# Optimization experiments

Measured on AMD Instinct MI355X. Metric: run time of the kernel, lower is better.

Reference implementation:

```python
import jax, jax.numpy as jnp
import numpy as np

B, K, U, I, D = 16384, 64, 100000, 100000, 256

def setup_inputs() -> dict:
    key = jax.random.key(0)
    k1, k2, k3, k4, k5, k6, k7, k8 = jax.random.split(key, 8)
    return {
        "nodes_u": jax.random.randint(k1, (B,), 0, U),
        "nodes_v": jax.random.randint(k2, (B,), 0, I),
        "neighbors": jax.random.randint(k3, (B, K), 0, U),
        "neighbor_counts": jax.random.randint(k4, (B,), 0, K + 1),
        "u2e": jax.random.normal(k5, (U, D), dtype=jnp.float32),
        "v2e": jax.random.normal(k6, (I, D), dtype=jnp.float32),
        "W": jax.random.normal(k7, (D, 2 * D), dtype=jnp.float32) * 0.05,  # torch Linear weight [out, in]
        "b": jax.random.normal(k8, (D,), dtype=jnp.float32) * 0.05,
    }

def reference(nodes_u, nodes_v, neighbors, neighbor_counts, u2e, v2e, W, b):
    # self embeddings [B, D]
    self_emb = u2e[nodes_u]
    # gather padded neighbor embeddings [B, K, D]
    neib_emb = u2e[neighbors]
    k_ = neighbors.shape[1]
    mask = jnp.arange(k_)[None, :] < neighbor_counts[:, None]          # [B, K] valid-neighbor mask
    nsum = jnp.einsum('bkd,bk->bd', neib_emb, mask.astype(neib_emb.dtype))
    cnt = jnp.maximum(neighbor_counts, 1).astype(self_emb.dtype)[:, None]
    nmean = nsum / cnt                                                  # mean-pool over valid neighbors
    cat = jnp.concatenate([self_emb, nmean], axis=1)                    # [B, 2D]
    proj = cat @ W.T + b                                                # Linear(2D -> D)
    # users with no neighbors use raw self embedding (matches `if len(neibs) > 0` branch)
    uemb = jnp.where((neighbor_counts > 0)[:, None], proj, self_emb)
    scores = jnp.sum(uemb * v2e[nodes_v], axis=1)                       # [B]
    return scores
```

## Files before the change

### kernel.cpp

```cpp
#include <hip/hip_runtime.h>
#include <hip/hip_fp16.h>

#define B_ROWS   16384
#define K_NB     64
#define U_ROWS   100000
#define D_DIM    256
#define TWO_D    512
#define R_BLK    8
#define THREADS  256

typedef float f32x2_t __attribute__((ext_vector_type(2)));

#if __has_builtin(__builtin_amdgcn_cvt_pk_f32_fp8) && __has_builtin(__builtin_amdgcn_cvt_pk_fp8_f32)
#define FP8_HW 1
#else
#define FP8_HW 0
#include <hip/hip_fp8.h>
#endif

__device__ __forceinline__ unsigned pack4_fp8(float a, float b, float c, float d) {
#if FP8_HW
    int v = 0;
    v = __builtin_amdgcn_cvt_pk_fp8_f32(a, b, v, false);
    v = __builtin_amdgcn_cvt_pk_fp8_f32(c, d, v, true);
    return (unsigned)v;
#else
    __hip_fp8_e4m3 x0(a), x1(b), x2(c), x3(d);
    return (unsigned)x0.__x | ((unsigned)x1.__x << 8)
         | ((unsigned)x2.__x << 16) | ((unsigned)x3.__x << 24);
#endif
}

__device__ __forceinline__ float4 unpack4_fp8(unsigned u) {
#if FP8_HW
    const f32x2_t lo = __builtin_amdgcn_cvt_pk_f32_fp8((int)u, false);
    const f32x2_t hi = __builtin_amdgcn_cvt_pk_f32_fp8((int)u, true);
    return make_float4(lo[0], lo[1], hi[0], hi[1]);
#else
    __hip_fp8_e4m3 x0, x1, x2, x3;
    x0.__x = u & 0xff; x1.__x = (u >> 8) & 0xff;
    x2.__x = (u >> 16) & 0xff; x3.__x = (u >> 24) & 0xff;
    return make_float4((float)x0, (float)x1, (float)x2, (float)x3);
#endif
}

__global__ __launch_bounds__(256)
void cvt_u2e_fp8(const float* __restrict__ src, uint2* __restrict__ dst, int n8) {
    const int i = blockIdx.x * 256 + threadIdx.x;
    if (i >= n8) return;
    const float4 a = ((const float4*)src)[2 * i];
    const float4 b = ((const float4*)src)[2 * i + 1];
    uint2 o;
    o.x = pack4_fp8(a.x, a.y, a.z, a.w);
    o.y = pack4_fp8(b.x, b.y, b.z, b.w);
    dst[i] = o;
}

__global__ __launch_bounds__(THREADS, 4)
void easyrec_fused_q(const int* __restrict__ nodes_u,
                     const int* __restrict__ nodes_v,
                     const int* __restrict__ neighbors,
                     const int* __restrict__ neighbor_counts,
                     const float* __restrict__ u2e,
                     const unsigned char* __restrict__ u8,
                     const float* __restrict__ v2e,
                     const float* __restrict__ W,
                     const float* __restrict__ bias,
                     float* __restrict__ out)
{
    __shared__ __align__(16) int   nbr_lds[R_BLK * K_NB];
    __shared__ __align__(16) float cat_lds[R_BLK][TWO_D];
    __shared__ float red_lds[R_BLK * 4];
    __shared__ float selfdot_lds[R_BLK];
    __shared__ float bdot_lds[R_BLK];

    const int t    = threadIdx.x;
    const int wave = t >> 6;
    const int lane = t & 63;
    const int row0 = blockIdx.x * R_BLK;

    nbr_lds[t]           = neighbors[(size_t)row0 * K_NB + t];
    nbr_lds[t + THREADS] = neighbors[(size_t)row0 * K_NB + t + THREADS];
    __syncthreads();

    const unsigned colb = (unsigned)lane * 16u;
    const unsigned colq = (unsigned)lane * 4u;

    {
        const float4 b4 = *(const float4*)((const char*)bias + colb);
        #pragma unroll
        for (int rr = 0; rr < 2; ++rr) {
            const int r   = wave + rr * 4;
            const int row = row0 + r;
            const int nu  = __builtin_amdgcn_readfirstlane(nodes_u[row]);
            const int nv  = __builtin_amdgcn_readfirstlane(nodes_v[row]);
            const float4 self4 = *(const float4*)((const char*)u2e + (((size_t)nu) << 10) + colb);
            const float4 v4    = *(const float4*)((const char*)v2e + (((size_t)nv) << 10) + colb);
            *(float4*)(&cat_lds[r][4 * lane]) = self4;
            float sv = self4.x * v4.x + self4.y * v4.y + self4.z * v4.z + self4.w * v4.w;
            float bv = b4.x * v4.x + b4.y * v4.y + b4.z * v4.z + b4.w * v4.w;
            #pragma unroll
            for (int off = 32; off > 0; off >>= 1) {
                sv += __shfl_xor(sv, off, 64);
                bv += __shfl_xor(bv, off, 64);
            }
            if (lane == 0) { selfdot_lds[r] = sv; bdot_lds[r] = bv; }
        }
    }

    const int rowA = row0 + wave, rowB = rowA + 4;
    const int cntA = __builtin_amdgcn_readfirstlane(neighbor_counts[rowA]);
    const int cntB = __builtin_amdgcn_readfirstlane(neighbor_counts[rowB]);
    const int itA = (cntA + 7) >> 3;
    const int itB = (cntB + 7) >> 3;
    const int itMin = itA < itB ? itA : itB;
    const int itMax = itA > itB ? itA : itB;
    const int baseA = wave * K_NB;
    const int baseB = baseA + 4 * K_NB;

#define LOADQ8(P, BASE, KK)                                                         \
    const int4 P##ia = *(const int4*)&nbr_lds[(BASE) + (KK)];                       \
    const int4 P##ib = *(const int4*)&nbr_lds[(BASE) + (KK) + 4];                   \
    const unsigned P##n0 = *(const unsigned*)(u8 + (((unsigned)P##ia.x) << 8) + colq); \
    const unsigned P##n1 = *(const unsigned*)(u8 + (((unsigned)P##ia.y) << 8) + colq); \
    const unsigned P##n2 = *(const unsigned*)(u8 + (((unsigned)P##ia.z) << 8) + colq); \
    const unsigned P##n3 = *(const unsigned*)(u8 + (((unsigned)P##ia.w) << 8) + colq); \
    const unsigned P##n4 = *(const unsigned*)(u8 + (((unsigned)P##ib.x) << 8) + colq); \
    const unsigned P##n5 = *(const unsigned*)(u8 + (((unsigned)P##ib.y) << 8) + colq); \
    const unsigned P##n6 = *(const unsigned*)(u8 + (((unsigned)P##ib.z) << 8) + colq); \
    const unsigned P##n7 = *(const unsigned*)(u8 + (((unsigned)P##ib.w) << 8) + colq);

#define ACCQ1(P, N, ACC, M)                                                         \
    {                                                                               \
        const float4 f = unpack4_fp8(P##N);                                         \
        ACC.x += (M) * f.x; ACC.y += (M) * f.y;                                     \
        ACC.z += (M) * f.z; ACC.w += (M) * f.w;                                     \
    }

#define ACCQ8(P, ACC, CNT, KK)                                                      \
    {                                                                               \
        const float m0 = ((KK) + 0 < (CNT)) ? 1.f : 0.f;                            \
        const float m1 = ((KK) + 1 < (CNT)) ? 1.f : 0.f;                            \
        const float m2 = ((KK) + 2 < (CNT)) ? 1.f : 0.f;                            \
        const float m3 = ((KK) + 3 < (CNT)) ? 1.f : 0.f;                            \
        const float m4 = ((KK) + 4 < (CNT)) ? 1.f : 0.f;                            \
        const float m5 = ((KK) + 5 < (CNT)) ? 1.f : 0.f;                            \
        const float m6 = ((KK) + 6 < (CNT)) ? 1.f : 0.f;                            \
        const float m7 = ((KK) + 7 < (CNT)) ? 1.f : 0.f;                            \
        ACCQ1(P, n0, ACC, m0) ACCQ1(P, n1, ACC, m1)                                 \
        ACCQ1(P, n2, ACC, m2) ACCQ1(P, n3, ACC, m3)                                 \
        ACCQ1(P, n4, ACC, m4) ACCQ1(P, n5, ACC, m5)                                 \
        ACCQ1(P, n6, ACC, m6) ACCQ1(P, n7, ACC, m7)                                 \
    }

    float4 accA = make_float4(0.f, 0.f, 0.f, 0.f);
    float4 accB = make_float4(0.f, 0.f, 0.f, 0.f);

    for (int i = 0; i < itMin; ++i) {
        const int k = i << 3;
        LOADQ8(A, baseA, k)
        LOADQ8(B, baseB, k)
        ACCQ8(A, accA, cntA, k)
        ACCQ8(B, accB, cntB, k)
    }
    if (itMin < itMax) {
        const bool Along = itA > itB;
        const int  cntL  = Along ? cntA : cntB;
        const int  baseL = Along ? baseA : baseB;
        float4 accL = make_float4(0.f, 0.f, 0.f, 0.f);
        for (int i = itMin; i < itMax; ++i) {
            const int k = i << 3;
            LOADQ8(L, baseL, k)
            ACCQ8(L, accL, cntL, k)
        }
        if (Along) {
            accA.x += accL.x; accA.y += accL.y; accA.z += accL.z; accA.w += accL.w;
        } else {
            accB.x += accL.x; accB.y += accL.y; accB.z += accL.z; accB.w += accL.w;
        }
    }
#undef LOADQ8
#undef ACCQ8
#undef ACCQ1

    {
        const float invA = 1.0f / (float)(cntA > 0 ? cntA : 1);
        const float invB = 1.0f / (float)(cntB > 0 ? cntB : 1);
        *(float4*)(&cat_lds[wave][D_DIM + 4 * lane]) =
            make_float4(accA.x * invA, accA.y * invA, accA.z * invA, accA.w * invA);
        *(float4*)(&cat_lds[wave + 4][D_DIM + 4 * lane]) =
            make_float4(accB.x * invB, accB.y * invB, accB.z * invB, accB.w * invB);
    }
    __syncthreads();

    unsigned voff[R_BLK];
    #pragma unroll
    for (int r = 0; r < R_BLK; ++r) {
        const int nv = __builtin_amdgcn_readfirstlane(nodes_v[row0 + r]);
        voff[r] = ((unsigned)nv) << 10;
    }

    float2 acc2[R_BLK];
    #pragma unroll
    for (int r = 0; r < R_BLK; ++r) acc2[r] = make_float2(0.f, 0.f);

    const unsigned tb8 = (unsigned)t * 8u;
    for (int d = 0; d < D_DIM; d += 4) {
        float4 vq[R_BLK];
        #pragma unroll
        for (int r = 0; r < R_BLK; ++r)
            vq[r] = *(const float4*)((const char*)v2e + voff[r] + (unsigned)d * 4u);

        #pragma unroll
        for (int dd = 0; dd < 4; ++dd) {
            const float2 wq = *(const float2*)((const char*)W + (((unsigned)(d + dd)) << 11) + tb8);
            #pragma unroll
            for (int r = 0; r < R_BLK; ++r) {
                const float vs = (dd == 0) ? vq[r].x : (dd == 1) ? vq[r].y
                               : (dd == 2) ? vq[r].z : vq[r].w;
                acc2[r].x += wq.x * vs;
                acc2[r].y += wq.y * vs;
            }
        }
    }

    #pragma unroll
    for (int r = 0; r < R_BLK; ++r) {
        const float2 c2 = *(const float2*)(&cat_lds[r][2 * t]);
        float p = c2.x * acc2[r].x + c2.y * acc2[r].y;
        #pragma unroll
        for (int off = 32; off > 0; off >>= 1) p += __shfl_xor(p, off, 64);
        if (lane == 0) red_lds[r * 4 + wave] = p;
    }
    __syncthreads();

    if (t < R_BLK) {
        const int row = row0 + t;
        const int cnt = neighbor_counts[row];
        float s;
        if (cnt > 0) {
            s = red_lds[t * 4 + 0] + red_lds[t * 4 + 1]
              + red_lds[t * 4 + 2] + red_lds[t * 4 + 3] + bdot_lds[t];
        } else {
            s = selfdot_lds[t];
        }
        out[row] = s;
    }
}

__global__ __launch_bounds__(THREADS, 4)
void easyrec_fused_f(const int* __restrict__ nodes_u,
                     const int* __restrict__ nodes_v,
                     const int* __restrict__ neighbors,
                     const int* __restrict__ neighbor_counts,
                     const float* __restrict__ u2e,
                     const float* __restrict__ v2e,
                     const float* __restrict__ W,
                     const float* __restrict__ bias,
                     float* __restrict__ out)
{
    __shared__ __align__(16) int   nbr_lds[R_BLK * K_NB];
    __shared__ __align__(16) float cat_lds[R_BLK][TWO_D];
    __shared__ float red_lds[R_BLK * 4];
    __shared__ float selfdot_lds[R_BLK];
    __shared__ float bdot_lds[R_BLK];

    const int t    = threadIdx.x;
    const int wave = t >> 6;
    const int lane = t & 63;
    const int row0 = blockIdx.x * R_BLK;

    nbr_lds[t]           = neighbors[(size_t)row0 * K_NB + t];
    nbr_lds[t + THREADS] = neighbors[(size_t)row0 * K_NB + t + THREADS];
    __syncthreads();

    for (int rr = 0; rr < 2; ++rr) {
        const int r   = wave + rr * 4;
        const int row = row0 + r;
        const int nu  = __builtin_amdgcn_readfirstlane(nodes_u[row]);
        const int nv  = __builtin_amdgcn_readfirstlane(nodes_v[row]);
        const int cnt = __builtin_amdgcn_readfirstlane(neighbor_counts[row]);

        const float4 self4 = *(const float4*)(u2e + (size_t)nu * D_DIM + 4 * lane);
        const float4 v4    = *(const float4*)(v2e + (size_t)nv * D_DIM + 4 * lane);
        const float4 b4    = *(const float4*)(bias + 4 * lane);

        float4 acc = make_float4(0.f, 0.f, 0.f, 0.f);
        const int base = r * K_NB;
        const int kmax = (cnt + 7) & ~7;
        for (int k = 0; k < kmax; k += 8) {
            const int4 ia = *(const int4*)&nbr_lds[base + k];
            const int4 ib = *(const int4*)&nbr_lds[base + k + 4];
            const float4 n0 = *(const float4*)(u2e + (size_t)ia.x * D_DIM + 4 * lane);
            const float4 n1 = *(const float4*)(u2e + (size_t)ia.y * D_DIM + 4 * lane);
            const float4 n2 = *(const float4*)(u2e + (size_t)ia.z * D_DIM + 4 * lane);
            const float4 n3 = *(const float4*)(u2e + (size_t)ia.w * D_DIM + 4 * lane);
            const float4 n4 = *(const float4*)(u2e + (size_t)ib.x * D_DIM + 4 * lane);
            const float4 n5 = *(const float4*)(u2e + (size_t)ib.y * D_DIM + 4 * lane);
            const float4 n6 = *(const float4*)(u2e + (size_t)ib.z * D_DIM + 4 * lane);
            const float4 n7 = *(const float4*)(u2e + (size_t)ib.w * D_DIM + 4 * lane);
            const float m0 = (k + 0 < cnt) ? 1.f : 0.f;
            const float m1 = (k + 1 < cnt) ? 1.f : 0.f;
            const float m2 = (k + 2 < cnt) ? 1.f : 0.f;
            const float m3 = (k + 3 < cnt) ? 1.f : 0.f;
            const float m4 = (k + 4 < cnt) ? 1.f : 0.f;
            const float m5 = (k + 5 < cnt) ? 1.f : 0.f;
            const float m6 = (k + 6 < cnt) ? 1.f : 0.f;
            const float m7 = (k + 7 < cnt) ? 1.f : 0.f;
            acc.x += n0.x*m0 + n1.x*m1 + n2.x*m2 + n3.x*m3 + n4.x*m4 + n5.x*m5 + n6.x*m6 + n7.x*m7;
            acc.y += n0.y*m0 + n1.y*m1 + n2.y*m2 + n3.y*m3 + n4.y*m4 + n5.y*m5 + n6.y*m6 + n7.y*m7;
            acc.z += n0.z*m0 + n1.z*m1 + n2.z*m2 + n3.z*m3 + n4.z*m4 + n5.z*m5 + n6.z*m6 + n7.z*m7;
            acc.w += n0.w*m0 + n1.w*m1 + n2.w*m2 + n3.w*m3 + n4.w*m4 + n5.w*m5 + n6.w*m6 + n7.w*m7;
        }
        const float inv = 1.0f / (float)(cnt > 0 ? cnt : 1);
        *(float4*)(&cat_lds[r][4 * lane])         = self4;
        *(float4*)(&cat_lds[r][D_DIM + 4 * lane]) =
            make_float4(acc.x * inv, acc.y * inv, acc.z * inv, acc.w * inv);

        float sv = self4.x * v4.x + self4.y * v4.y + self4.z * v4.z + self4.w * v4.w;
        float bv = b4.x * v4.x + b4.y * v4.y + b4.z * v4.z + b4.w * v4.w;
        #pragma unroll
        for (int off = 32; off > 0; off >>= 1) {
            sv += __shfl_xor(sv, off, 64);
            bv += __shfl_xor(bv, off, 64);
        }
        if (lane == 0) { selfdot_lds[r] = sv; bdot_lds[r] = bv; }
    }
    __syncthreads();

    const float* vrow[R_BLK];
    #pragma unroll
    for (int r = 0; r < R_BLK; ++r) {
        const int nv = __builtin_amdgcn_readfirstlane(nodes_v[row0 + r]);
        vrow[r] = v2e + (size_t)nv * D_DIM;
    }

    float2 acc2[R_BLK];
    #pragma unroll
    for (int r = 0; r < R_BLK; ++r) acc2[r] = make_float2(0.f, 0.f);

    for (int d = 0; d < D_DIM; d += 4) {
        float4 vq[R_BLK];
        #pragma unroll
        for (int r = 0; r < R_BLK; ++r) vq[r] = *(const float4*)(vrow[r] + d);
        #pragma unroll
        for (int dd = 0; dd < 4; ++dd) {
            const float2 wq = *(const float2*)(W + (size_t)(d + dd) * TWO_D + 2 * t);
            #pragma unroll
            for (int r = 0; r < R_BLK; ++r) {
                const float vs = (dd == 0) ? vq[r].x : (dd == 1) ? vq[r].y
                               : (dd == 2) ? vq[r].z : vq[r].w;
                acc2[r].x += wq.x * vs;
                acc2[r].y += wq.y * vs;
            }
        }
    }

    #pragma unroll
    for (int r = 0; r < R_BLK; ++r) {
        const float2 c2 = *(const float2*)(&cat_lds[r][2 * t]);
        float p = c2.x * acc2[r].x + c2.y * acc2[r].y;
        #pragma unroll
        for (int off = 32; off > 0; off >>= 1) p += __shfl_xor(p, off, 64);
        if (lane == 0) red_lds[r * 4 + wave] = p;
    }
    __syncthreads();

    if (t < R_BLK) {
        const int row = row0 + t;
        const int cnt = neighbor_counts[row];
        float s;
        if (cnt > 0) {
            s = red_lds[t * 4 + 0] + red_lds[t * 4 + 1]
              + red_lds[t * 4 + 2] + red_lds[t * 4 + 3] + bdot_lds[t];
        } else {
            s = selfdot_lds[t];
        }
        out[row] = s;
    }
}

extern "C" void kernel_launch(void* const* d_in, const int* in_sizes, int n_in,
                              void* d_out, int out_size, void* d_ws, size_t ws_size,
                              hipStream_t stream) {
    const int*   nodes_u         = (const int*)d_in[0];
    const int*   nodes_v         = (const int*)d_in[1];
    const int*   neighbors       = (const int*)d_in[2];
    const int*   neighbor_counts = (const int*)d_in[3];
    const float* u2e             = (const float*)d_in[4];
    const float* v2e             = (const float*)d_in[5];
    const float* W               = (const float*)d_in[6];
    const float* bias            = (const float*)d_in[7];
    float*       out             = (float*)d_out;

    const size_t need = (size_t)U_ROWS * D_DIM;
    const int blocks = B_ROWS / R_BLK;

    if (d_ws != nullptr && ws_size >= need) {
        unsigned char* u8 = (unsigned char*)d_ws;
        const int n8 = U_ROWS * D_DIM / 8;
        const int cblocks = (n8 + 255) / 256;
        cvt_u2e_fp8<<<cblocks, 256, 0, stream>>>(u2e, (uint2*)u8, n8);
        easyrec_fused_q<<<blocks, THREADS, 0, stream>>>(
            nodes_u, nodes_v, neighbors, neighbor_counts, u2e, u8, v2e, W, bias, out);
    } else {
        easyrec_fused_f<<<blocks, THREADS, 0, stream>>>(
            nodes_u, nodes_v, neighbors, neighbor_counts, u2e, v2e, W, bias, out);
    }
}
```

Baseline: 302.6 us.

## Specialize waves: two gather neighbors while two compute W-projection concurrently

```diff
diff --git a/kernel.cpp b/kernel.cpp
--- a/kernel.cpp
+++ b/kernel.cpp
@@ -70,7 +70,7 @@
 {
     __shared__ __align__(16) int   nbr_lds[R_BLK * K_NB];
     __shared__ __align__(16) float cat_lds[R_BLK][TWO_D];
-    __shared__ float red_lds[R_BLK * 4];
+    __shared__ float red_lds[R_BLK * 2];
     __shared__ float selfdot_lds[R_BLK];
     __shared__ float bdot_lds[R_BLK];
 
@@ -83,40 +83,31 @@
     nbr_lds[t + THREADS] = neighbors[(size_t)row0 * K_NB + t + THREADS];
     __syncthreads();
 
-    const unsigned colb = (unsigned)lane * 16u;
-    const unsigned colq = (unsigned)lane * 4u;
-
-    {
-        const float4 b4 = *(const float4*)((const char*)bias + colb);
-        #pragma unroll
-        for (int rr = 0; rr < 2; ++rr) {
-            const int r   = wave + rr * 4;
-            const int row = row0 + r;
-            const int nu  = __builtin_amdgcn_readfirstlane(nodes_u[row]);
-            const int nv  = __builtin_amdgcn_readfirstlane(nodes_v[row]);
-            const float4 self4 = *(const float4*)((const char*)u2e + (((size_t)nu) << 10) + colb);
-            const float4 v4    = *(const float4*)((const char*)v2e + (((size_t)nv) << 10) + colb);
-            *(float4*)(&cat_lds[r][4 * lane]) = self4;
-            float sv = self4.x * v4.x + self4.y * v4.y + self4.z * v4.z + self4.w * v4.w;
-            float bv = b4.x * v4.x + b4.y * v4.y + b4.z * v4.z + b4.w * v4.w;
+    if (wave < 2) {
+        const unsigned colb = (unsigned)lane * 16u;
+        const unsigned colq = (unsigned)lane * 4u;
+
+        {
+            const float4 b4 = *(const float4*)((const char*)bias + colb);
             #pragma unroll
-            for (int off = 32; off > 0; off >>= 1) {
-                sv += __shfl_xor(sv, off, 64);
-                bv += __shfl_xor(bv, off, 64);
+            for (int rr = 0; rr < 4; ++rr) {
+                const int r   = wave * 2 + (rr & 1) + (rr >> 1) * 4;
+                const int row = row0 + r;
+                const int nu  = __builtin_amdgcn_readfirstlane(nodes_u[row]);
+                const int nv  = __builtin_amdgcn_readfirstlane(nodes_v[row]);
+                const float4 self4 = *(const float4*)((const char*)u2e + (((size_t)nu) << 10) + colb);
+                const float4 v4    = *(const float4*)((const char*)v2e + (((size_t)nv) << 10) + colb);
+                *(float4*)(&cat_lds[r][4 * lane]) = self4;
+                float sv = self4.x * v4.x + self4.y * v4.y + self4.z * v4.z + self4.w * v4.w;
+                float bv = b4.x * v4.x + b4.y * v4.y + b4.z * v4.z + b4.w * v4.w;
+                #pragma unroll
+                for (int off = 32; off > 0; off >>= 1) {
+                    sv += __shfl_xor(sv, off, 64);
+                    bv += __shfl_xor(bv, off, 64);
+                }
+                if (lane == 0) { selfdot_lds[r] = sv; bdot_lds[r] = bv; }
             }
-            if (lane == 0) { selfdot_lds[r] = sv; bdot_lds[r] = bv; }
-        }
-    }
-
-    const int rowA = row0 + wave, rowB = rowA + 4;
-    const int cntA = __builtin_amdgcn_readfirstlane(neighbor_counts[rowA]);
-    const int cntB = __builtin_amdgcn_readfirstlane(neighbor_counts[rowB]);
-    const int itA = (cntA + 7) >> 3;
-    const int itB = (cntB + 7) >> 3;
-    const int itMin = itA < itB ? itA : itB;
-    const int itMax = itA > itB ? itA : itB;
-    const int baseA = wave * K_NB;
-    const int baseB = baseA + 4 * K_NB;
+        }
 
 #define LOADQ8(P, BASE, KK)                                                         \
     const int4 P##ia = *(const int4*)&nbr_lds[(BASE) + (KK)];                       \
@@ -153,85 +144,103 @@
         ACCQ1(P, n6, ACC, m6) ACCQ1(P, n7, ACC, m7)                                 \
     }
 
-    float4 accA = make_float4(0.f, 0.f, 0.f, 0.f);
-    float4 accB = make_float4(0.f, 0.f, 0.f, 0.f);
-
-    for (int i = 0; i < itMin; ++i) {
-        const int k = i << 3;
-        LOADQ8(A, baseA, k)
-        LOADQ8(B, baseB, k)
-        ACCQ8(A, accA, cntA, k)
-        ACCQ8(B, accB, cntB, k)
-    }
-    if (itMin < itMax) {
-        const bool Along = itA > itB;
-        const int  cntL  = Along ? cntA : cntB;
-        const int  baseL = Along ? baseA : baseB;
-        float4 accL = make_float4(0.f, 0.f, 0.f, 0.f);
-        for (int i = itMin; i < itMax; ++i) {
-            const int k = i << 3;
-            LOADQ8(L, baseL, k)
-            ACCQ8(L, accL, cntL, k)
-        }
-        if (Along) {
-            accA.x += accL.x; accA.y += accL.y; accA.z += accL.z; accA.w += accL.w;
-        } else {
-            accB.x += accL.x; accB.y += accL.y; accB.z += accL.z; accB.w += accL.w;
-        }
-    }
+        for (int pp = 0; pp < 2; ++pp) {
+            const int rA = wave * 2 + pp;
+            const int rB = rA + 4;
+            const int cntA = __builtin_amdgcn_readfirstlane(neighbor_counts[row0 + rA]);
+            const int cntB = __builtin_amdgcn_readfirstlane(neighbor_counts[row0 + rB]);
+            const int itA = (cntA + 7) >> 3;
+            const int itB = (cntB + 7) >> 3;
+            const int itMin = itA < itB ? itA : itB;
+            const int itMax = itA > itB ? itA : itB;
+            const int baseA = rA * K_NB;
+            const int baseB = rB * K_NB;
+
+            float4 accA = make_float4(0.f, 0.f, 0.f, 0.f);
+            float4 accB = make_float4(0.f, 0.f, 0.f, 0.f);
+
+            for (int i = 0; i < itMin; ++i) {
+                const int k = i << 3;
+                LOADQ8(A, baseA, k)
+                LOADQ8(B, baseB, k)
+                ACCQ8(A, accA, cntA, k)
+                ACCQ8(B, accB, cntB, k)
+            }
+            if (itMin < itMax) {
+                const bool Along = itA > itB;
+                const int  cntL  = Along ? cntA : cntB;
+                const int  baseL = Along ? baseA : baseB;
+                float4 accL = make_float4(0.f, 0.f, 0.f, 0.f);
+                for (int i = itMin; i < itMax; ++i) {
+                    const int k = i << 3;
+                    LOADQ8(L, baseL, k)
+                    ACCQ8(L, accL, cntL, k)
+                }
+                if (Along) {
+                    accA.x += accL.x; accA.y += accL.y; accA.z += accL.z; accA.w += accL.w;
+                } else {
+                    accB.x += accL.x; accB.y += accL.y; accB.z += accL.z; accB.w += accL.w;
+                }
+            }
+
+            const float invA = 1.0f / (float)(cntA > 0 ? cntA : 1);
+            const float invB = 1.0f / (float)(cntB > 0 ? cntB : 1);
+            *(float4*)(&cat_lds[rA][D_DIM + 4 * lane]) =
+                make_float4(accA.x * invA, accA.y * invA, accA.z * invA, accA.w * invA);
+            *(float4*)(&cat_lds[rB][D_DIM + 4 * lane]) =
+                make_float4(accB.x * invB, accB.y * invB, accB.z * invB, accB.w * invB);
+        }
 #undef LOADQ8
 #undef ACCQ8
 #undef ACCQ1
-
-    {
-        const float invA = 1.0f / (float)(cntA > 0 ? cntA : 1);
-        const float invB = 1.0f / (float)(cntB > 0 ? cntB : 1);
-        *(float4*)(&cat_lds[wave][D_DIM + 4 * lane]) =
-            make_float4(accA.x * invA, accA.y * invA, accA.z * invA, accA.w * invA);
-        *(float4*)(&cat_lds[wave + 4][D_DIM + 4 * lane]) =
-            make_float4(accB.x * invB, accB.y * invB, accB.z * invB, accB.w * invB);
-    }
-    __syncthreads();
-
-    unsigned voff[R_BLK];
-    #pragma unroll
-    for (int r = 0; r < R_BLK; ++r) {
-        const int nv = __builtin_amdgcn_readfirstlane(nodes_v[row0 + r]);
-        voff[r] = ((unsigned)nv) << 10;
-    }
-
-    float2 acc2[R_BLK];
-    #pragma unroll
-    for (int r = 0; r < R_BLK; ++r) acc2[r] = make_float2(0.f, 0.f);
-
-    const unsigned tb8 = (unsigned)t * 8u;
-    for (int d = 0; d < D_DIM; d += 4) {
-        float4 vq[R_BLK];
-        #pragma unroll
-        for (int r = 0; r < R_BLK; ++r)
-            vq[r] = *(const float4*)((const char*)v2e + voff[r] + (unsigned)d * 4u);
-
-        #pragma unroll
-        for (int dd = 0; dd < 4; ++dd) {
-            const float2 wq = *(const float2*)((const char*)W + (((unsigned)(d + dd)) << 11) + tb8);
+    } else {
+        const int tm = t - 128;
+        unsigned voff[R_BLK];
+        #pragma unroll
+        for (int r = 0; r < R_BLK; ++r) {
+            const int nv = __builtin_amdgcn_readfirstlane(nodes_v[row0 + r]);
+            voff[r] = ((unsigned)nv) << 10;
+        }
+
+        float4 acc4[R_BLK];
+        #pragma unroll
+        for (int r = 0; r < R_BLK; ++r) acc4[r] = make_float4(0.f, 0.f, 0.f, 0.f);
+
+        const unsigned tb16 = (unsigned)tm * 16u;
+        for (int d = 0; d < D_DIM; d += 4) {
+            float4 vq[R_BLK];
             #pragma unroll
-            for (int r = 0; r < R_BLK; ++r) {
-                const float vs = (dd == 0) ? vq[r].x : (dd == 1) ? vq[r].y
-                               : (dd == 2) ? vq[r].z : vq[r].w;
-                acc2[r].x += wq.x * vs;
-                acc2[r].y += wq.y * vs;
+            for (int r = 0; r < R_BLK; ++r)
+                vq[r] = *(const float4*)((const char*)v2e + voff[r] + (unsigned)d * 4u);
+
+            #pragma unroll
+            for (int dd = 0; dd < 4; ++dd) {
+                const float4 w4 = *(const float4*)((const char*)W + (((unsigned)(d + dd)) << 11) + tb16);
+                #pragma unroll
+                for (int r = 0; r < R_BLK; ++r) {
+                    const float vs = (dd == 0) ? vq[r].x : (dd == 1) ? vq[r].y
+                                   : (dd == 2) ? vq[r].z : vq[r].w;
+                    acc4[r].x += w4.x * vs;
+                    acc4[r].y += w4.y * vs;
+                    acc4[r].z += w4.z * vs;
+                    acc4[r].w += w4.w * vs;
+                }
             }
         }
-    }
-
-    #pragma unroll
-    for (int r = 0; r < R_BLK; ++r) {
-        const float2 c2 = *(const float2*)(&cat_lds[r][2 * t]);
-        float p = c2.x * acc2[r].x + c2.y * acc2[r].y;
-        #pragma unroll
-        for (int off = 32; off > 0; off >>= 1) p += __shfl_xor(p, off, 64);
-        if (lane == 0) red_lds[r * 4 + wave] = p;
-    }
+        __syncthreads();
+
+        #pragma unroll
+        for (int r = 0; r < R_BLK; ++r) {
+            const float4 c4 = *(const float4*)(&cat_lds[r][4 * tm]);
+            float p = c4.x * acc4[r].x + c4.y * acc4[r].y
+                    + c4.z * acc4[r].z + c4.w * acc4[r].w;
+            #pragma unroll
+            for (int off = 32; off > 0; off >>= 1) p += __shfl_xor(p, off, 64);
+            if (lane == 0) red_lds[r * 2 + (wave - 2)] = p;
+        }
+    }
+
+    if (wave < 2) __syncthreads();
     __syncthreads();
 
     if (t < R_BLK) {
@@ -239,8 +248,7 @@
         const int cnt = neighbor_counts[row];
         float s;
         if (cnt > 0) {
-            s = red_lds[t * 4 + 0] + red_lds[t * 4 + 1]
-              + red_lds[t * 4 + 2] + red_lds[t * 4 + 3] + bdot_lds[t];
+            s = red_lds[t * 2 + 0] + red_lds[t * 2 + 1] + bdot_lds[t];
         } else {
             s = selfdot_lds[t];
         }
```

Result: faster. 292.3 us (-3.4%).
